# Optimization experiments

Hardware: AMD Instinct MI355X
Metric: run time of the kernel (lower is better)

Reference implementation:

```python
import jax, jax.numpy as jnp
import numpy as np

B, P, EPG = 1000, 100, 1200  # graphs, nodes/graph, edges/graph
IN, HID, OUT, K = 16, 64, 5, 3


def setup_inputs() -> dict:
    key = jax.random.key(0)
    ks = jax.random.split(key, 12)
    offs = jnp.repeat(jnp.arange(B, dtype=jnp.int32) * P, EPG)
    src = jax.random.randint(ks[0], (B * EPG,), 0, P, dtype=jnp.int32) + offs
    dst = jax.random.randint(ks[1], (B * EPG,), 0, P, dtype=jnp.int32) + offs
    graph_ids = jnp.repeat(jnp.arange(B, dtype=jnp.int32), P)
    feat = jax.random.normal(ks[2], (B * P, IN), dtype=jnp.float32)

    def lin(k1, fan_in, fan_out):
        s = 1.0 / np.sqrt(fan_in)
        return jax.random.uniform(k1, (fan_in, fan_out), jnp.float32, -s, s)

    return {
        'feat': feat, 'src': src, 'dst': dst, 'graph_ids': graph_ids,
        'n_graphs': B,
        'W1': lin(ks[3], K * IN, HID), 'b1': jnp.zeros((HID,), jnp.float32),
        'W2': lin(ks[4], K * HID, HID), 'b2': jnp.zeros((HID,), jnp.float32),
        'W3': lin(ks[5], K * HID, HID), 'b3': jnp.zeros((HID,), jnp.float32),
        'Wfc': lin(ks[6], HID, OUT), 'bfc': jnp.zeros((OUT,), jnp.float32),
    }


def _cheb_conv(x, src, dst, d_invsqrt, W, b, k):
    # DGL ChebConv with lambda_max=2 -> re_norm=1, scaled Laplacian = -D^-1/2 A D^-1/2
    n = x.shape[0]

    def Ax(h):
        msg = (h * d_invsqrt)[src]                      # gather from source nodes
        agg = jax.ops.segment_sum(msg, dst, num_segments=n)
        return agg * d_invsqrt

    Xs = [x]
    if k > 1:
        Xs.append(-Ax(Xs[0]))                           # X1 = L_hat X0
        for _ in range(2, k):
            Xs.append(-2.0 * Ax(Xs[-1]) - Xs[-2])       # X_i = 2 L_hat X_{i-1} - X_{i-2}
    Xt = jnp.concatenate(Xs, axis=1)                    # [n, k*f]
    return Xt @ W + b


def reference(feat, src, dst, graph_ids, n_graphs, W1, b1, W2, b2, W3, b3, Wfc, bfc):
    n = feat.shape[0]
    deg = jax.ops.segment_sum(jnp.ones((src.shape[0],), feat.dtype), dst, num_segments=n)
    d_invsqrt = jnp.where(deg < 1.0, 1.0, deg) ** -0.5
    d_invsqrt = d_invsqrt[:, None]

    h = jax.nn.relu(_cheb_conv(feat, src, dst, d_invsqrt, W1, b1, K))
    h = jax.nn.relu(_cheb_conv(h, src, dst, d_invsqrt, W2, b2, K))
    h = jax.nn.relu(_cheb_conv(h, src, dst, d_invsqrt, W3, b3, K))

    # dgl.mean_nodes: per-graph mean pooling
    counts = jax.ops.segment_sum(jnp.ones((n,), h.dtype), graph_ids, num_segments=n_graphs)
    hg = jax.ops.segment_sum(h, graph_ids, num_segments=n_graphs) / counts[:, None]
    return hg @ Wfc + bfc
```

## Files before the change

kernel.cpp:

```cpp
#include <hip/hip_runtime.h>

#define NGRAPH 1000
#define P      100
#define EPG    1200
#define INF    16
#define HID    64
#define NOUT   5

#define ASTR   88
#define T2OFF  72
#define SLOTA  64
#define SLOTB  80
#define NPAD   112


typedef short short8 __attribute__((ext_vector_type(8)));
typedef float f32x4  __attribute__((ext_vector_type(4)));

__device__ __forceinline__ void bsplit(float x, short& h, short& l) {
    unsigned u = __float_as_uint(x);
    h = (short)(u >> 16);
    float hf = __uint_as_float(u & 0xffff0000u);
    l = (short)(__float_as_uint(x - hf) >> 16);
}

__global__ __launch_bounds__(256) void wprep(
    const float* __restrict__ W1, const float* __restrict__ W2,
    const float* __restrict__ W3, short* __restrict__ wt)
{
    const int i0 = blockIdx.x * blockDim.x + threadIdx.x;
    const int stride = gridDim.x * blockDim.x;
    for (int e = i0; e < HID * 56; e += stride) {
        int c = e / 56, r = e % 56;
        float v = (r < 48) ? W1[r * HID + c] : 0.f;
        short h, l; bsplit(v, h, l);
        wt[e]        = h;
        wt[3584 + e] = l;
    }
    for (int e = i0; e < HID * 200; e += stride) {
        int c = e / 200, r = e % 200;
        float v2 = (r < 192) ? W2[r * HID + c] : 0.f;
        float v3 = (r < 192) ? W3[r * HID + c] : 0.f;
        short h, l;
        bsplit(v2, h, l); wt[7168 + e]  = h; wt[19968 + e] = l;
        bsplit(v3, h, l); wt[32768 + e] = h; wt[45568 + e] = l;
    }
}

__device__ __forceinline__ void prop_x1(
    float* __restrict__ A, int soff, int dslot,
    const unsigned char* __restrict__ csr_src,
    const int* __restrict__ csr_off,
    const float* __restrict__ dinv, int tid)
{
    const int q4 = (tid & 1) * 4;
    const int n  = tid >> 1;
    if (n < P) {
        const int kb = csr_off[n], ke = csr_off[n + 1];
        float ax = 0.f, ay = 0.f, az = 0.f, aw = 0.f;
        for (int k = kb; k < ke; k++) {
            int s = csr_src[k];
            const float4 x = *(const float4*)&A[s * ASTR + soff + q4];
            ax += x.x; ay += x.y; az += x.z; aw += x.w;
        }
        float dn = dinv[n];
        float m = -dn * dn;
        float4 o; o.x = m * ax; o.y = m * ay; o.z = m * az; o.w = m * aw;
        *(float4*)&A[n * ASTR + dslot + q4] = o;
    }
}

__device__ __forceinline__ void prop_dual(
    float* __restrict__ A, int t1c, int t1n, int ycur, int ynext, bool pre,
    const unsigned char* __restrict__ csr_src,
    const int* __restrict__ csr_off,
    const float* __restrict__ dinv, int tid)
{
    const int q4 = (tid & 1) * 4;
    const int n  = tid >> 1;
    if (n < P) {
        const int kb = csr_off[n], ke = csr_off[n + 1];
        float4 a2 = make_float4(0.f, 0.f, 0.f, 0.f);
        float4 a1 = make_float4(0.f, 0.f, 0.f, 0.f);
        if (pre) {
            for (int k = kb; k < ke; k++) {
                int s = csr_src[k];
                const float* rp = &A[s * ASTR + q4];
                const float4 x2 = *(const float4*)&rp[t1c];
                const float4 x1 = *(const float4*)&rp[ynext];
                a2.x += x2.x; a2.y += x2.y; a2.z += x2.z; a2.w += x2.w;
                a1.x += x1.x; a1.y += x1.y; a1.z += x1.z; a1.w += x1.w;
            }
        } else {
            for (int k = kb; k < ke; k++) {
                int s = csr_src[k];
                const float4 x2 = *(const float4*)&A[s * ASTR + t1c + q4];
                a2.x += x2.x; a2.y += x2.y; a2.z += x2.z; a2.w += x2.w;
            }
        }
        float dn = dinv[n];
        float d2 = dn * dn;
        const float4 y0 = *(const float4*)&A[n * ASTR + ycur + q4];
        float4 o2;
        float m2 = -2.f * d2;
        o2.x = m2 * a2.x - y0.x; o2.y = m2 * a2.y - y0.y;
        o2.z = m2 * a2.z - y0.z; o2.w = m2 * a2.w - y0.w;
        *(float4*)&A[n * ASTR + T2OFF + q4] = o2;
        if (pre) {
            float m1 = -d2;
            float4 o1;
            o1.x = m1 * a1.x; o1.y = m1 * a1.y;
            o1.z = m1 * a1.z; o1.w = m1 * a1.w;
            *(float4*)&A[n * ASTR + t1n + q4] = o1;
        }
    }
}

template <int F, int FINAL>
__device__ __forceinline__ void cheb_layer(
    float* __restrict__ A,
    const unsigned char* __restrict__ csr_src,
    const int* __restrict__ csr_off,
    const float* __restrict__ dinv,
    const short* __restrict__ whi, const short* __restrict__ wlo,
    const float* __restrict__ bias, int tid)
{
    const int RK   = 3 * F + 8;
    const int lane = tid & 63;
    const int wv   = tid >> 6;
    const int n16  = lane & 15;
    const int q    = lane >> 4;
    const int ncol = (wv << 4) + n16;

    f32x4 acc[7];
#pragma unroll
    for (int t = 0; t < 7; t++) { acc[t][0]=0.f; acc[t][1]=0.f; acc[t][2]=0.f; acc[t][3]=0.f; }

    prop_x1(A, 0, SLOTA, csr_src, csr_off, dinv, tid);
    __syncthreads();

    int t1c = SLOTA, t1n = SLOTB;
    for (int cb = 0; cb < F; cb += 8) {
        const bool pre = (cb + 8 < F);
        prop_dual(A, t1c, t1n, cb, cb + 8, pre, csr_src, csr_off, dinv, tid);
        __syncthreads();

        const int wr = (q == 0) ? cb : (q == 1) ? (F + cb)
                     : (q == 2) ? (2 * F + cb) : (3 * F);
        const short8 bhi = *(const short8*)&whi[ncol * RK + wr];
        const short8 blo = *(const short8*)&wlo[ncol * RK + wr];

        const int aoff = (q == 0) ? cb : (q == 1) ? t1c
                       : (q == 2) ? T2OFF : cb;
#pragma unroll
        for (int t = 0; t < 7; t++) {
            const float* xp = &A[(t * 16 + n16) * ASTR + aoff];
            const float4 v0 = *(const float4*)xp;
            const float4 v1 = *(const float4*)(xp + 4);
            short8 ahi, alo; short h, l;
            bsplit(v0.x, h, l); ahi[0] = h; alo[0] = l;
            bsplit(v0.y, h, l); ahi[1] = h; alo[1] = l;
            bsplit(v0.z, h, l); ahi[2] = h; alo[2] = l;
            bsplit(v0.w, h, l); ahi[3] = h; alo[3] = l;
            bsplit(v1.x, h, l); ahi[4] = h; alo[4] = l;
            bsplit(v1.y, h, l); ahi[5] = h; alo[5] = l;
            bsplit(v1.z, h, l); ahi[6] = h; alo[6] = l;
            bsplit(v1.w, h, l); ahi[7] = h; alo[7] = l;
            acc[t] = __builtin_amdgcn_mfma_f32_16x16x32_bf16(ahi, bhi, acc[t], 0, 0, 0);
            acc[t] = __builtin_amdgcn_mfma_f32_16x16x32_bf16(ahi, blo, acc[t], 0, 0, 0);
            acc[t] = __builtin_amdgcn_mfma_f32_16x16x32_bf16(alo, bhi, acc[t], 0, 0, 0);
        }
        __syncthreads();
        int tt = t1c; t1c = t1n; t1n = tt;
    }

    const float bcol = bias[ncol];
    const int rbase = q * 4;
#pragma unroll
    for (int t = 0; t < 7; t++) {
#pragma unroll
        for (int r = 0; r < 4; r++) {
            int row = t * 16 + rbase + r;
            if (row < P) {
                float dn = dinv[row];
                float v = acc[t][r];
                float o;
                if (FINAL) o = fmaxf(v * (1.0f / dn) + bcol, 0.f);
                else       o = fmaxf(v + bcol * dn, 0.f);
                A[row * ASTR + ncol] = o;
            }
        }
    }
    __syncthreads();
}

__global__ __launch_bounds__(256, 4) void gnn_kernel(
    const float* __restrict__ feat,
    const int* __restrict__ src, const int* __restrict__ dst,
    const float* __restrict__ b1, const float* __restrict__ b2,
    const float* __restrict__ b3,
    const float* __restrict__ Wfc, const float* __restrict__ bfc,
    const short* __restrict__ wt,
    float* __restrict__ out)
{
    __shared__ __align__(16) float A[NPAD * ASTR];
    __shared__ unsigned char csr_src[EPG];

    const int g = blockIdx.x;
    const int tid = threadIdx.x;
    const int base = g * P;
    const int* srcg = src + g * EPG;
    const int* dstg = dst + g * EPG;

    int*   deg     = (int*)&A[P * ASTR];
    int*   cur     = (int*)&A[P * ASTR + 100];
    int*   csr_off = (int*)&A[P * ASTR + 200];
    float* dinv    = &A[P * ASTR + 304];
    float* psum    = &A[P * ASTR + 404];

    for (int i = tid; i < P; i += 256) deg[i] = 0;
    __syncthreads();
    for (int e = tid; e < EPG; e += 256) {
        int d = dstg[e] - base;
        atomicAdd(&deg[d], 1);
    }
    __syncthreads();

    for (int i = tid; i < P; i += 256) {
        int dg = deg[i] > 1 ? deg[i] : 1;
        dinv[i] = rsqrtf((float)dg);
    }
    if (tid == 0) {
        int run = 0;
        csr_off[0] = 0;
        for (int i = 0; i < P; i++) { run += deg[i]; csr_off[i + 1] = run; }
    }
    __syncthreads();

    for (int i = tid; i < P * INF / 4; i += 256) {
        int n = i >> 2, fq = (i & 3) * 4;
        float4 v = *(const float4*)&feat[(size_t)base * INF + i * 4];
        float dn = dinv[n];
        v.x *= dn; v.y *= dn; v.z *= dn; v.w *= dn;
        *(float4*)&A[n * ASTR + fq] = v;
    }
    for (int i = tid; i < P; i += 256) cur[i] = csr_off[i];
    __syncthreads();
    for (int e = tid; e < EPG; e += 256) {
        int s = srcg[e] - base;
        int d = dstg[e] - base;
        int pos = atomicAdd(&cur[d], 1);
        csr_src[pos] = (unsigned char)s;
    }
    __syncthreads();

    cheb_layer<INF, 0>(A, csr_src, csr_off, dinv, wt,         wt + 3584,  b1, tid);
    cheb_layer<HID, 0>(A, csr_src, csr_off, dinv, wt + 7168,  wt + 19968, b2, tid);
    cheb_layer<HID, 1>(A, csr_src, csr_off, dinv, wt + 32768, wt + 45568, b3, tid);

    {
        const int lane = tid & 63, w = tid >> 6;
        float s = 0.f;
        for (int n = w; n < P; n += 4) s += A[n * ASTR + lane];
        psum[w * 64 + lane] = s;
    }
    __syncthreads();
    if (tid < HID) {
        float hg = (psum[tid] + psum[64 + tid] + psum[128 + tid] + psum[192 + tid]) * (1.0f / P);
        psum[256 + tid] = hg;
    }
    __syncthreads();
    if (tid < NOUT) {
        float o = bfc[tid];
        for (int c = 0; c < HID; c++) o += psum[256 + c] * Wfc[c * NOUT + tid];
        out[g * NOUT + tid] = o;
    }
}

extern "C" void kernel_launch(void* const* d_in, const int* in_sizes, int n_in,
                              void* d_out, int out_size, void* d_ws, size_t ws_size,
                              hipStream_t stream)
{
    const float* feat = (const float*)d_in[0];
    const int*   src  = (const int*)d_in[1];
    const int*   dst  = (const int*)d_in[2];
    const float* W1  = (const float*)d_in[5];
    const float* b1  = (const float*)d_in[6];
    const float* W2  = (const float*)d_in[7];
    const float* b2  = (const float*)d_in[8];
    const float* W3  = (const float*)d_in[9];
    const float* b3  = (const float*)d_in[10];
    const float* Wfc = (const float*)d_in[11];
    const float* bfc = (const float*)d_in[12];
    float* out = (float*)d_out;
    short* wt = (short*)d_ws;

    wprep<<<64, 256, 0, stream>>>(W1, W2, W3, wt);
    gnn_kernel<<<NGRAPH, 256, 0, stream>>>(feat, src, dst,
                                           b1, b2, b3, Wfc, bfc, wt, out);
}
```

Baseline: 186.0 us.

## Degree-sort nodes and split heavy nodes across idle lanes in propagation

Node gathers were split evenly: 200 threads, two per node, while 56 threads sat idle. Now one thread counting-sorts nodes by degree (descending), and each wave takes 25 nodes in that order. The 14 spare lanes per wave take the tail edges of the 7 highest-degree nodes, and the partial sums are merged with a shuffle. This is meant to balance per-wave gather loop lengths and cut the warp divergence caused by uneven degrees. The cost is serial single-thread sorting during setup (overlapped with CSR fill), extra shuffles, and a per-wave cap heuristic.

```diff
diff --git a/kernel.cpp b/kernel.cpp
--- a/kernel.cpp
+++ b/kernel.cpp
@@ -50,68 +50,77 @@
 __device__ __forceinline__ void prop_x1(
     float* __restrict__ A, int soff, int dslot,
     const unsigned char* __restrict__ csr_src,
-    const int* __restrict__ csr_off,
-    const float* __restrict__ dinv, int tid)
-{
-    const int q4 = (tid & 1) * 4;
-    const int n  = tid >> 1;
-    if (n < P) {
-        const int kb = csr_off[n], ke = csr_off[n + 1];
-        float ax = 0.f, ay = 0.f, az = 0.f, aw = 0.f;
-        for (int k = kb; k < ke; k++) {
-            int s = csr_src[k];
-            const float4 x = *(const float4*)&A[s * ASTR + soff + q4];
-            ax += x.x; ay += x.y; az += x.z; aw += x.w;
-        }
-        float dn = dinv[n];
+    int nn, int kb, int ke, int q4, float dn, int lane)
+{
+    float ax = 0.f, ay = 0.f, az = 0.f, aw = 0.f;
+    for (int k = kb; k < ke; k++) {
+        int s = csr_src[k];
+        const float4 x = *(const float4*)&A[s * ASTR + soff + q4];
+        ax += x.x; ay += x.y; az += x.z; aw += x.w;
+    }
+    float p0 = __shfl(ax, (lane + 50) & 63);
+    float p1 = __shfl(ay, (lane + 50) & 63);
+    float p2 = __shfl(az, (lane + 50) & 63);
+    float p3 = __shfl(aw, (lane + 50) & 63);
+    if (lane < 14) { ax += p0; ay += p1; az += p2; aw += p3; }
+    if (lane < 50) {
         float m = -dn * dn;
         float4 o; o.x = m * ax; o.y = m * ay; o.z = m * az; o.w = m * aw;
-        *(float4*)&A[n * ASTR + dslot + q4] = o;
+        *(float4*)&A[nn * ASTR + dslot + q4] = o;
     }
 }
 
 __device__ __forceinline__ void prop_dual(
     float* __restrict__ A, int t1c, int t1n, int ycur, int ynext, bool pre,
     const unsigned char* __restrict__ csr_src,
-    const int* __restrict__ csr_off,
-    const float* __restrict__ dinv, int tid)
-{
-    const int q4 = (tid & 1) * 4;
-    const int n  = tid >> 1;
-    if (n < P) {
-        const int kb = csr_off[n], ke = csr_off[n + 1];
-        float4 a2 = make_float4(0.f, 0.f, 0.f, 0.f);
-        float4 a1 = make_float4(0.f, 0.f, 0.f, 0.f);
-        if (pre) {
-            for (int k = kb; k < ke; k++) {
-                int s = csr_src[k];
-                const float* rp = &A[s * ASTR + q4];
-                const float4 x2 = *(const float4*)&rp[t1c];
-                const float4 x1 = *(const float4*)&rp[ynext];
-                a2.x += x2.x; a2.y += x2.y; a2.z += x2.z; a2.w += x2.w;
-                a1.x += x1.x; a1.y += x1.y; a1.z += x1.z; a1.w += x1.w;
-            }
-        } else {
-            for (int k = kb; k < ke; k++) {
-                int s = csr_src[k];
-                const float4 x2 = *(const float4*)&A[s * ASTR + t1c + q4];
-                a2.x += x2.x; a2.y += x2.y; a2.z += x2.z; a2.w += x2.w;
-            }
-        }
-        float dn = dinv[n];
+    int nn, int kb, int ke, int q4, float dn, int lane)
+{
+    float4 a2 = make_float4(0.f, 0.f, 0.f, 0.f);
+    float4 a1 = make_float4(0.f, 0.f, 0.f, 0.f);
+    if (pre) {
+        for (int k = kb; k < ke; k++) {
+            int s = csr_src[k];
+            const float* rp = &A[s * ASTR + q4];
+            const float4 x2 = *(const float4*)&rp[t1c];
+            const float4 x1 = *(const float4*)&rp[ynext];
+            a2.x += x2.x; a2.y += x2.y; a2.z += x2.z; a2.w += x2.w;
+            a1.x += x1.x; a1.y += x1.y; a1.z += x1.z; a1.w += x1.w;
+        }
+    } else {
+        for (int k = kb; k < ke; k++) {
+            int s = csr_src[k];
+            const float4 x2 = *(const float4*)&A[s * ASTR + t1c + q4];
+            a2.x += x2.x; a2.y += x2.y; a2.z += x2.z; a2.w += x2.w;
+        }
+    }
+    {
+        float p0 = __shfl(a2.x, (lane + 50) & 63);
+        float p1 = __shfl(a2.y, (lane + 50) & 63);
+        float p2 = __shfl(a2.z, (lane + 50) & 63);
+        float p3 = __shfl(a2.w, (lane + 50) & 63);
+        if (lane < 14) { a2.x += p0; a2.y += p1; a2.z += p2; a2.w += p3; }
+    }
+    if (pre) {
+        float p0 = __shfl(a1.x, (lane + 50) & 63);
+        float p1 = __shfl(a1.y, (lane + 50) & 63);
+        float p2 = __shfl(a1.z, (lane + 50) & 63);
+        float p3 = __shfl(a1.w, (lane + 50) & 63);
+        if (lane < 14) { a1.x += p0; a1.y += p1; a1.z += p2; a1.w += p3; }
+    }
+    if (lane < 50) {
         float d2 = dn * dn;
-        const float4 y0 = *(const float4*)&A[n * ASTR + ycur + q4];
+        const float4 y0 = *(const float4*)&A[nn * ASTR + ycur + q4];
+        float m2 = -2.f * d2;
         float4 o2;
-        float m2 = -2.f * d2;
         o2.x = m2 * a2.x - y0.x; o2.y = m2 * a2.y - y0.y;
         o2.z = m2 * a2.z - y0.z; o2.w = m2 * a2.w - y0.w;
-        *(float4*)&A[n * ASTR + T2OFF + q4] = o2;
+        *(float4*)&A[nn * ASTR + T2OFF + q4] = o2;
         if (pre) {
             float m1 = -d2;
             float4 o1;
             o1.x = m1 * a1.x; o1.y = m1 * a1.y;
             o1.z = m1 * a1.z; o1.w = m1 * a1.w;
-            *(float4*)&A[n * ASTR + t1n + q4] = o1;
+            *(float4*)&A[nn * ASTR + t1n + q4] = o1;
         }
     }
 }
@@ -122,12 +131,27 @@
     const unsigned char* __restrict__ csr_src,
     const int* __restrict__ csr_off,
     const float* __restrict__ dinv,
+    const unsigned char* __restrict__ order,
+    const int* __restrict__ Tw,
     const short* __restrict__ whi, const short* __restrict__ wlo,
     const float* __restrict__ bias, int tid)
 {
     const int RK   = 3 * F + 8;
     const int lane = tid & 63;
     const int wv   = tid >> 6;
+
+    int slot, gq;
+    if (lane < 50) { slot = lane >> 1;        gq = lane & 1; }
+    else           { slot = (lane - 50) >> 1; gq = (lane - 50) & 1; }
+    const int nn  = order[wv * 25 + slot];
+    const int kb0 = csr_off[nn], ke0 = csr_off[nn + 1];
+    const int tw  = Tw[wv];
+    const int cap = (kb0 + tw < ke0) ? kb0 + tw : ke0;
+    const int gkb = (lane < 50) ? kb0 : cap;
+    const int gke = (lane < 50) ? cap : ke0;
+    const int gq4 = gq * 4;
+    const float gdn = dinv[nn];
+
     const int n16  = lane & 15;
     const int q    = lane >> 4;
     const int ncol = (wv << 4) + n16;
@@ -136,13 +160,14 @@
 #pragma unroll
     for (int t = 0; t < 7; t++) { acc[t][0]=0.f; acc[t][1]=0.f; acc[t][2]=0.f; acc[t][3]=0.f; }
 
-    prop_x1(A, 0, SLOTA, csr_src, csr_off, dinv, tid);
+    prop_x1(A, 0, SLOTA, csr_src, nn, gkb, gke, gq4, gdn, lane);
     __syncthreads();
 
     int t1c = SLOTA, t1n = SLOTB;
     for (int cb = 0; cb < F; cb += 8) {
         const bool pre = (cb + 8 < F);
-        prop_dual(A, t1c, t1n, cb, cb + 8, pre, csr_src, csr_off, dinv, tid);
+        prop_dual(A, t1c, t1n, cb, cb + 8, pre, csr_src,
+                  nn, gkb, gke, gq4, gdn, lane);
         __syncthreads();
 
         const int wr = (q == 0) ? cb : (q == 1) ? (F + cb)
@@ -182,11 +207,11 @@
         for (int r = 0; r < 4; r++) {
             int row = t * 16 + rbase + r;
             if (row < P) {
-                float dn = dinv[row];
+                float dnr = dinv[row];
                 float v = acc[t][r];
                 float o;
-                if (FINAL) o = fmaxf(v * (1.0f / dn) + bcol, 0.f);
-                else       o = fmaxf(v + bcol * dn, 0.f);
+                if (FINAL) o = fmaxf(v * (1.0f / dnr) + bcol, 0.f);
+                else       o = fmaxf(v + bcol * dnr, 0.f);
                 A[row * ASTR + ncol] = o;
             }
         }
@@ -217,6 +242,8 @@
     int*   csr_off = (int*)&A[P * ASTR + 200];
     float* dinv    = &A[P * ASTR + 304];
     float* psum    = &A[P * ASTR + 404];
+    unsigned char* order = (unsigned char*)&A[P * ASTR + 724];
+    int*   Tw      = (int*)&A[P * ASTR + 750];
 
     for (int i = tid; i < P; i += 256) deg[i] = 0;
     __syncthreads();
@@ -246,17 +273,31 @@
     }
     for (int i = tid; i < P; i += 256) cur[i] = csr_off[i];
     __syncthreads();
-    for (int e = tid; e < EPG; e += 256) {
-        int s = srcg[e] - base;
-        int d = dstg[e] - base;
-        int pos = atomicAdd(&cur[d], 1);
-        csr_src[pos] = (unsigned char)s;
-    }
-    __syncthreads();
-
-    cheb_layer<INF, 0>(A, csr_src, csr_off, dinv, wt,         wt + 3584,  b1, tid);
-    cheb_layer<HID, 0>(A, csr_src, csr_off, dinv, wt + 7168,  wt + 19968, b2, tid);
-    cheb_layer<HID, 1>(A, csr_src, csr_off, dinv, wt + 32768, wt + 45568, b3, tid);
+
+    if (tid < 255) {
+        for (int e = tid; e < EPG; e += 255) {
+            int s = srcg[e] - base;
+            int d = dstg[e] - base;
+            int pos = atomicAdd(&cur[d], 1);
+            csr_src[pos] = (unsigned char)s;
+        }
+    } else {
+        int* bucket = (int*)psum;
+        for (int i = 0; i < 64; i++) bucket[i] = 0;
+        for (int i = 0; i < P; i++) { int d = deg[i] < 63 ? deg[i] : 63; bucket[d]++; }
+        int run = 0;
+        for (int d = 63; d >= 0; d--) { int c = bucket[d]; bucket[d] = run; run += c; }
+        for (int i = 0; i < P; i++) {
+            int d = deg[i] < 63 ? deg[i] : 63;
+            order[bucket[d]++] = (unsigned char)i;
+        }
+        for (int w = 0; w < 4; w++) Tw[w] = deg[order[w * 25 + 7]];
+    }
+    __syncthreads();
+
+    cheb_layer<INF, 0>(A, csr_src, csr_off, dinv, order, Tw, wt,         wt + 3584,  b1, tid);
+    cheb_layer<HID, 0>(A, csr_src, csr_off, dinv, order, Tw, wt + 7168,  wt + 19968, b2, tid);
+    cheb_layer<HID, 1>(A, csr_src, csr_off, dinv, order, Tw, wt + 32768, wt + 45568, b3, tid);
 
     {
         const int lane = tid & 63, w = tid >> 6;
```

After: 190.8 us. 2.5% more time.
